# Performance work log

Measured on AMD Instinct MI355X. Metric: run time of the kernel, lower is better.

## Reference

```python
import jax, jax.numpy as jnp
import numpy as np

B, T, C = 128, 256, 384
H, HD = 8, 48          # num_heads, head_dim
WINDOW = 64

def setup_inputs() -> dict:
    key = jax.random.key(0)
    ks = jax.random.split(key, 5)
    return {
        "x": jax.random.normal(ks[0], (B, T, C), dtype=jnp.float32),
        "W_qkv": jax.random.normal(ks[1], (C, 3 * C), dtype=jnp.float32) * (1.0 / np.sqrt(C)),
        "b_qkv": jax.random.normal(ks[2], (3 * C,), dtype=jnp.float32) * 0.02,
        "W_proj": jax.random.normal(ks[3], (C, C), dtype=jnp.float32) * (1.0 / np.sqrt(C)),
        "b_proj": jax.random.normal(ks[4], (C,), dtype=jnp.float32) * 0.02,
        "gate": jnp.ones((C,), dtype=jnp.float32),
    }

def reference(x, W_qkv, b_qkv, W_proj, b_proj, gate):
    Bx, Tx, Cx = x.shape
    qkv = x @ W_qkv + b_qkv                                   # [B,T,3C]
    q, k, v = jnp.split(qkv, 3, axis=-1)
    q = q.reshape(Bx, Tx, H, HD).transpose(0, 2, 1, 3)        # [B,H,T,hd]
    k = k.reshape(Bx, Tx, H, HD).transpose(0, 2, 1, 3)
    v = v.reshape(Bx, Tx, H, HD).transpose(0, 2, 1, 3)
    scale = 1.0 / np.sqrt(HD).astype(np.float32)
    att = jnp.einsum("bhqd,bhkd->bhqk", q, k) * scale        # [B,H,T,T]
    idx = jnp.arange(Tx)
    causal = idx[:, None] >= idx[None, :]                     # lower-tri
    local = jnp.abs(idx[None, :] - idx[:, None]) <= WINDOW
    mask = (causal & local)[None, None, :, :]
    att = jnp.where(mask, att, -jnp.inf)
    att = jax.nn.softmax(att, axis=-1)
    out = jnp.einsum("bhqk,bhkd->bhqd", att, v)               # [B,H,T,hd]
    out = out.transpose(0, 2, 1, 3).reshape(Bx, Tx, Cx)       # [B,T,C]
    return (out * gate) @ W_proj + b_proj
```

## Files before the change

kernel.cpp:

```cpp
#include <hip/hip_runtime.h>
#include <hip/hip_bf16.h>

typedef __attribute__((ext_vector_type(8))) short bf16x8;
typedef __attribute__((ext_vector_type(4))) float floatx4;

#define NB 128
#define NT 256
#define NC 384
#define NH 8
#define ND 48
#define CPLANE (128 * 8 * 256 * 48)

static __device__ __forceinline__ unsigned short f2bf(float f) {
  __hip_bfloat16 h = __float2bfloat16(f);
  return __builtin_bit_cast(unsigned short, h);
}

static __device__ __forceinline__ void gload16(const unsigned short* g, unsigned short* l) {
  __builtin_amdgcn_global_load_lds(
      (const __attribute__((address_space(1))) void*)g,
      (__attribute__((address_space(3))) void*)l, 16, 0, 0);
}

__global__ __launch_bounds__(256) void k_prep(const float* __restrict__ x,
                                              const float* __restrict__ Wq,
                                              const float* __restrict__ Wp,
                                              const float* __restrict__ gate,
                                              unsigned short* __restrict__ xbf,
                                              unsigned short* __restrict__ WqT,
                                              unsigned short* __restrict__ WpT) {
  const int blk = blockIdx.x;
  const int t = threadIdx.x;
  if (blk < 144) {
    __shared__ float T[64][65];
    const float* src;
    unsigned short* dst;
    int N, kt, nt;
    const bool isWp = (blk >= 108);
    if (!isWp) { src = Wq; dst = WqT; N = 1152; kt = blk / 18; nt = blk % 18; }
    else { int b2 = blk - 108; src = Wp; dst = WpT; N = 384; kt = b2 / 6; nt = b2 % 6; }
    const int k0 = kt * 64, n0 = nt * 64;
    const int r = t >> 2, c = (t & 3) * 16;
    const float* s = src + (size_t)(k0 + r) * N + n0 + c;
#pragma unroll
    for (int i = 0; i < 4; ++i) *(float4*)&T[r][c + i * 4] = ((const float4*)s)[i];
    __syncthreads();
    float gv[16];
    if (isWp) {
#pragma unroll
      for (int i = 0; i < 4; ++i) *(float4*)&gv[i * 4] = ((const float4*)(gate + k0 + c))[i];
    } else {
#pragma unroll
      for (int i = 0; i < 16; ++i) gv[i] = 1.f;
    }
    unsigned short o[16];
#pragma unroll
    for (int i = 0; i < 16; ++i) o[i] = f2bf(T[c + i][r] * gv[i]);
    unsigned short* dp = dst + (size_t)(n0 + r) * 384 + k0 + c;
    *(bf16x8*)dp = *(bf16x8*)&o[0];
    *(bf16x8*)(dp + 8) = *(bf16x8*)&o[8];
  } else {
    const int n8 = (NB * NT * NC) / 8;
    int idx = (blk - 144) * 256 + t;
    const int stride = (gridDim.x - 144) * 256;
    for (; idx < n8; idx += stride) {
      const float* s = x + (size_t)idx * 8;
      float v[8];
      *(float4*)&v[0] = ((const float4*)s)[0];
      *(float4*)&v[4] = ((const float4*)s)[1];
      bf16x8 p;
#pragma unroll
      for (int i = 0; i < 8; ++i) p[i] = f2bf(v[i]);
      *(bf16x8*)(xbf + (size_t)idx * 8) = p;
    }
  }
}

#define STAGE_G(Ag, Bg, k0, buf)                                                     \
  {                                                                                  \
    const int r0_ = (lane >> 2), sw0_ = 8 * ((lane & 3) ^ ((r0_ >> 1) & 3));         \
    const int r1_ = r0_ + 16,    sw1_ = 8 * ((lane & 3) ^ ((r1_ >> 1) & 3));         \
    gload16((Ag) + (size_t)r0_ * 384 + (k0) + sw0_, As + (buf)*4096 + (w * 32) * 32);  \
    gload16((Ag) + (size_t)r1_ * 384 + (k0) + sw1_, As + (buf)*4096 + (w * 32 + 16) * 32); \
    gload16((Bg) + (size_t)r0_ * 384 + (k0) + sw0_, Bs + (buf)*4096 + (w * 32) * 32);  \
    gload16((Bg) + (size_t)r1_ * 384 + (k0) + sw1_, Bs + (buf)*4096 + (w * 32 + 16) * 32); \
  }

#define GEMM_PIPE(Ag, Bg)                                                            \
  STAGE_G(Ag, Bg, 0, 0);                                                             \
  STAGE_G(Ag, Bg, 32, 1);                                                            \
  _Pragma("unroll") for (int t_ = 0; t_ < 12; ++t_) {                                \
    if (t_ < 11) asm volatile("s_waitcnt vmcnt(4)" ::: "memory");                    \
    else         asm volatile("s_waitcnt vmcnt(0)" ::: "memory");                    \
    __builtin_amdgcn_s_barrier();                                                    \
    if (t_ < 10) STAGE_G(Ag, Bg, (t_ + 2) * 32, (t_ + 2) % 3);                       \
    const unsigned short* Ac_ = As + (t_ % 3) * 4096;                                \
    const unsigned short* Bc_ = Bs + (t_ % 3) * 4096;                                \
    bf16x8 a_[4], b_[4];                                                             \
    _Pragma("unroll") for (int mt = 0; mt < 4; ++mt) {                               \
      const int R = wm * 64 + mt * 16 + lq;                                          \
      a_[mt] = *(const bf16x8*)&Ac_[R * 32 + 8 * (lg ^ ((R >> 1) & 3))];             \
    }                                                                                \
    _Pragma("unroll") for (int nt = 0; nt < 4; ++nt) {                               \
      const int R = wn * 64 + nt * 16 + lq;                                          \
      b_[nt] = *(const bf16x8*)&Bc_[R * 32 + 8 * (lg ^ ((R >> 1) & 3))];             \
    }                                                                                \
    _Pragma("unroll") for (int mt = 0; mt < 4; ++mt)                                 \
      _Pragma("unroll") for (int nt = 0; nt < 4; ++nt)                               \
        acc[mt][nt] = __builtin_amdgcn_mfma_f32_16x16x32_bf16(a_[mt], b_[nt], acc[mt][nt], 0, 0, 0); \
  }

__global__ __launch_bounds__(256) void k_qkv(const unsigned short* __restrict__ xb,
                                             const unsigned short* __restrict__ WqT,
                                             const float* __restrict__ bq,
                                             unsigned short* __restrict__ qkv) {
  __shared__ __align__(16) unsigned short As[3 * 4096];
  __shared__ __align__(16) unsigned short Bs[3 * 4096];
  const int t = threadIdx.x, lane = t & 63, w = t >> 6;
  const int wm = w >> 1, wn = w & 1;
  const int lq = lane & 15, lg = lane >> 4;
  const int swz = (blockIdx.x & 7) * 288 + (blockIdx.x >> 3);
  const int m0 = (swz / 9) * 128, n0 = (swz % 9) * 128;
  const int comp = n0 / 384;
  const unsigned short* Ag = xb + (size_t)(m0 + w * 32) * 384;
  const unsigned short* Bg = WqT + (size_t)(n0 + w * 32) * 384;
  floatx4 acc[4][4] = {};

  GEMM_PIPE(Ag, Bg);

  __builtin_amdgcn_s_barrier();
  unsigned short* Ew = ((w < 2) ? As : Bs) + 2 * 4096 + (w & 1) * 2048;
#pragma unroll
  for (int p = 0; p < 4; ++p) {
#pragma unroll
    for (int nt = 0; nt < 4; ++nt) {
      const float bias = bq[n0 + wn * 64 + nt * 16 + lq];
#pragma unroll
      for (int j = 0; j < 4; ++j)
        Ew[(lg * 4 + j) * 72 + nt * 16 + lq] = f2bf(acc[p][nt][j] + bias);
    }
    asm volatile("s_waitcnt lgkmcnt(0)" ::: "memory");
    __builtin_amdgcn_sched_barrier(0);
#pragma unroll
    for (int cc = 0; cc < 2; ++cc) {
      const int c = cc * 64 + lane;
      const int r16 = c >> 3, k8 = c & 7;
      bf16x8 v = *(const bf16x8*)&Ew[r16 * 72 + k8 * 8];
      const int lc = n0 - comp * 384 + wn * 64 + k8 * 8;
      const int hh = lc / 48, d0 = lc - hh * 48;
      const int R = m0 + wm * 64 + p * 16 + r16;
      *(bf16x8*)(qkv + (size_t)comp * CPLANE +
                 (((size_t)((R >> 8) * 8 + hh) * 256 + (R & 255)) * 48 + d0)) = v;
    }
    asm volatile("s_waitcnt lgkmcnt(0)" ::: "memory");
    __builtin_amdgcn_sched_barrier(0);
  }
}

__global__ __launch_bounds__(256) void k_proj(const unsigned short* __restrict__ A,
                                              const unsigned short* __restrict__ WpT,
                                              const float* __restrict__ bp,
                                              float* __restrict__ out) {
  __shared__ __align__(16) unsigned short As[3 * 4096];
  __shared__ __align__(16) unsigned short Bs[3 * 4096];
  const int t = threadIdx.x, lane = t & 63, w = t >> 6;
  const int wm = w >> 1, wn = w & 1;
  const int lq = lane & 15, lg = lane >> 4;
  const int swz = (blockIdx.x & 7) * 96 + (blockIdx.x >> 3);
  const int m0 = (swz / 3) * 128, n0 = (swz % 3) * 128;
  const unsigned short* Ag = A + (size_t)(m0 + w * 32) * 384;
  const unsigned short* Bg = WpT + (size_t)(n0 + w * 32) * 384;
  floatx4 acc[4][4] = {};

  GEMM_PIPE(Ag, Bg);

#pragma unroll
  for (int nt = 0; nt < 4; ++nt) {
    const int col = n0 + wn * 64 + nt * 16 + lq;
    const float bias = bp[col];
#pragma unroll
    for (int mt = 0; mt < 4; ++mt)
#pragma unroll
      for (int j = 0; j < 4; ++j) {
        const int row = m0 + wm * 64 + mt * 16 + lg * 4 + j;
        out[(size_t)row * 384 + col] = acc[mt][nt][j] + bias;
      }
  }
}

__global__ __launch_bounds__(256) void k_attn(const unsigned short* __restrict__ qkv,
                                              unsigned short* __restrict__ attg) {
  __shared__ __align__(16) unsigned short Ks[128 * 72];
  __shared__ __align__(16) unsigned short Vt[48 * 152];
  __shared__ __align__(16) unsigned short Ps[4 * 16 * 104];
  const int t = threadIdx.x;
  const int blk = blockIdx.x;
  const int tile = blk & 3;
  const int bh = blk >> 2;
  const int b = bh >> 3, h = bh & 7;
  const int base = tile * 64;
  const size_t kvoff = (size_t)bh * NT * ND;
  const unsigned short* qptr = qkv + kvoff;
  const unsigned short* kptr = qkv + (size_t)CPLANE + kvoff;
  const unsigned short* vptr = qkv + (size_t)2 * CPLANE + kvoff;

  if (t < 48) {
    bf16x8 z = {};
    *(bf16x8*)&Vt[t * 152 + 128] = z;
    *(bf16x8*)&Vt[t * 152 + 136] = z;
  }
  if (t < 128) {
    const int r = t, ka = base - 64 + r;
    unsigned short* dst = &Ks[r * 72];
    if (ka >= 0) {
      const unsigned short* src = kptr + (size_t)ka * ND;
#pragma unroll
      for (int i = 0; i < 6; ++i) *(bf16x8*)(dst + i * 8) = *(const bf16x8*)(src + i * 8);
      bf16x8 z = {};
      *(bf16x8*)(dst + 48) = z;
      *(bf16x8*)(dst + 56) = z;
    } else {
      bf16x8 z = {};
#pragma unroll
      for (int i = 0; i < 8; ++i) *(bf16x8*)(dst + i * 8) = z;
    }
  } else {
    const int r = t - 128, ka = base - 64 + r;
    if (ka >= 0) {
      const unsigned short* src = vptr + (size_t)ka * ND;
      bf16x8 vv[6];
#pragma unroll
      for (int i = 0; i < 6; ++i) vv[i] = *(const bf16x8*)(src + i * 8);
#pragma unroll
      for (int i = 0; i < 6; ++i)
#pragma unroll
        for (int j = 0; j < 8; ++j)
          Vt[(i * 8 + j) * 152 + r] = (unsigned short)vv[i][j];
    } else {
#pragma unroll
      for (int d = 0; d < 48; ++d) Vt[d * 152 + r] = 0;
    }
  }
  __syncthreads();

  const int lane = t & 63, w = t >> 6;
  const int lq = lane & 15, lg = lane >> 4;
  const int qs = base + w * 16;

  const unsigned short* qrow = qptr + (size_t)(qs + lq) * ND;
  bf16x8 aq0 = *(const bf16x8*)(qrow + lg * 8);
  bf16x8 aq1 = {};
  if (lg < 2) aq1 = *(const bf16x8*)(qrow + 32 + lg * 8);

  floatx4 s[5];
#pragma unroll
  for (int kt = 0; kt < 5; ++kt) {
    const unsigned short* kr = &Ks[(w * 16 + kt * 16 + lq) * 72];
    bf16x8 kb0 = *(const bf16x8*)(kr + lg * 8);
    bf16x8 kb1 = *(const bf16x8*)(kr + 32 + lg * 8);
    floatx4 z = {};
    z = __builtin_amdgcn_mfma_f32_16x16x32_bf16(aq0, kb0, z, 0, 0, 0);
    z = __builtin_amdgcn_mfma_f32_16x16x32_bf16(aq1, kb1, z, 0, 0, 0);
    s[kt] = z;
  }

  const float scale = 0.14433756729740643f;
  floatx4 pj[5];
#pragma unroll
  for (int j = 0; j < 4; ++j) {
    const int qa = qs + lg * 4 + j;
    float mx = -1e30f;
    float sv[5];
    bool ok[5];
#pragma unroll
    for (int kt = 0; kt < 5; ++kt) {
      const int ka = base - 64 + w * 16 + kt * 16 + lq;
      sv[kt] = s[kt][j] * scale;
      ok[kt] = (ka >= 0) && (ka <= qa) && (qa - ka <= 64);
      if (ok[kt]) mx = fmaxf(mx, sv[kt]);
    }
#pragma unroll
    for (int dd = 1; dd < 16; dd <<= 1) mx = fmaxf(mx, __shfl_xor(mx, dd));
    float sum = 0.f;
#pragma unroll
    for (int kt = 0; kt < 5; ++kt) {
      float p = ok[kt] ? __expf(sv[kt] - mx) : 0.f;
      pj[kt][j] = p;
      sum += p;
    }
#pragma unroll
    for (int dd = 1; dd < 16; dd <<= 1) sum += __shfl_xor(sum, dd);
    const float inv = 1.f / sum;
#pragma unroll
    for (int kt = 0; kt < 5; ++kt) pj[kt][j] *= inv;
  }

  unsigned short* pw = &Ps[w * 16 * 104];
#pragma unroll
  for (int kt = 0; kt < 5; ++kt)
#pragma unroll
    for (int j = 0; j < 4; ++j)
      pw[(lg * 4 + j) * 104 + kt * 16 + lq] = f2bf(pj[kt][j]);
#pragma unroll
  for (int j = 0; j < 4; ++j) pw[lq * 104 + 80 + lg * 4 + j] = 0;

  floatx4 o[3] = {};
#pragma unroll
  for (int c = 0; c < 3; ++c) {
    bf16x8 ap = *(const bf16x8*)&pw[lq * 104 + c * 32 + lg * 8];
#pragma unroll
    for (int nt = 0; nt < 3; ++nt) {
      bf16x8 av = *(const bf16x8*)&Vt[(nt * 16 + lq) * 152 + w * 16 + c * 32 + lg * 8];
      o[nt] = __builtin_amdgcn_mfma_f32_16x16x32_bf16(ap, av, o[nt], 0, 0, 0);
    }
  }
#pragma unroll
  for (int nt = 0; nt < 3; ++nt) {
    const int d = nt * 16 + lq;
    const int c = h * ND + d;
#pragma unroll
    for (int j = 0; j < 4; ++j) {
      const int tt = qs + lg * 4 + j;
      attg[((size_t)b * NT + tt) * NC + c] = f2bf(o[nt][j]);
    }
  }
}

extern "C" void kernel_launch(void* const* d_in, const int* in_sizes, int n_in,
                              void* d_out, int out_size, void* d_ws, size_t ws_size,
                              hipStream_t stream) {
  const float* x    = (const float*)d_in[0];
  const float* Wq   = (const float*)d_in[1];
  const float* bq   = (const float*)d_in[2];
  const float* Wp   = (const float*)d_in[3];
  const float* bp   = (const float*)d_in[4];
  const float* gate = (const float*)d_in[5];

  const size_t nx = (size_t)NB * NT * NC;
  unsigned short* attg = (unsigned short*)d_ws;
  unsigned short* xbf  = attg + nx;
  unsigned short* qkvp = xbf + nx;
  unsigned short* WqT  = qkvp + (size_t)3 * CPLANE;
  unsigned short* WpT  = WqT + (size_t)384 * 1152;
  float* out = (float*)d_out;

  k_prep<<<dim3(1680), 256, 0, stream>>>(x, Wq, Wp, gate, xbf, WqT, WpT);
  k_qkv<<<dim3(2304), 256, 0, stream>>>(xbf, WqT, bq, qkvp);
  k_attn<<<dim3(4096), 256, 0, stream>>>(qkvp, attg);
  k_proj<<<dim3(768), 256, 0, stream>>>(attg, WpT, bp, out);
}
```

Before: 113.3 us.

## Process whole sequence per (batch,head) block in attention, loading K/V once

The attention kernel now launches one block per (batch, head) instead of four per (batch, head) query tile. The full 256-row K and transposed V are loaded into shared memory once, and the block loops over four 64-row query segments. This removes the overlapping K/V window reloads and the zero-padding branches of the old 128-row staging. In exchange, shared memory per block grows and there are a quarter as many blocks, which lowers parallelism and occupancy.

```diff
diff --git a/kernel.cpp b/kernel.cpp
--- a/kernel.cpp
+++ b/kernel.cpp
@@ -190,139 +190,128 @@
 
 __global__ __launch_bounds__(256) void k_attn(const unsigned short* __restrict__ qkv,
                                               unsigned short* __restrict__ attg) {
-  __shared__ __align__(16) unsigned short Ks[128 * 72];
-  __shared__ __align__(16) unsigned short Vt[48 * 152];
+  __shared__ __align__(16) unsigned short Ks[256 * 72];
+  __shared__ __align__(16) unsigned short Vt[48 * 280];
   __shared__ __align__(16) unsigned short Ps[4 * 16 * 104];
   const int t = threadIdx.x;
-  const int blk = blockIdx.x;
-  const int tile = blk & 3;
-  const int bh = blk >> 2;
+  const int bh = blockIdx.x;
   const int b = bh >> 3, h = bh & 7;
-  const int base = tile * 64;
   const size_t kvoff = (size_t)bh * NT * ND;
   const unsigned short* qptr = qkv + kvoff;
   const unsigned short* kptr = qkv + (size_t)CPLANE + kvoff;
   const unsigned short* vptr = qkv + (size_t)2 * CPLANE + kvoff;
 
-  if (t < 48) {
+  {
+    const unsigned short* src = kptr + (size_t)t * ND;
+    unsigned short* dst = &Ks[t * 72];
+#pragma unroll
+    for (int i = 0; i < 6; ++i) *(bf16x8*)(dst + i * 8) = *(const bf16x8*)(src + i * 8);
     bf16x8 z = {};
-    *(bf16x8*)&Vt[t * 152 + 128] = z;
-    *(bf16x8*)&Vt[t * 152 + 136] = z;
-  }
-  if (t < 128) {
-    const int r = t, ka = base - 64 + r;
-    unsigned short* dst = &Ks[r * 72];
-    if (ka >= 0) {
-      const unsigned short* src = kptr + (size_t)ka * ND;
-#pragma unroll
-      for (int i = 0; i < 6; ++i) *(bf16x8*)(dst + i * 8) = *(const bf16x8*)(src + i * 8);
-      bf16x8 z = {};
-      *(bf16x8*)(dst + 48) = z;
-      *(bf16x8*)(dst + 56) = z;
-    } else {
-      bf16x8 z = {};
-#pragma unroll
-      for (int i = 0; i < 8; ++i) *(bf16x8*)(dst + i * 8) = z;
-    }
-  } else {
-    const int r = t - 128, ka = base - 64 + r;
-    if (ka >= 0) {
-      const unsigned short* src = vptr + (size_t)ka * ND;
-      bf16x8 vv[6];
-#pragma unroll
-      for (int i = 0; i < 6; ++i) vv[i] = *(const bf16x8*)(src + i * 8);
-#pragma unroll
-      for (int i = 0; i < 6; ++i)
-#pragma unroll
-        for (int j = 0; j < 8; ++j)
-          Vt[(i * 8 + j) * 152 + r] = (unsigned short)vv[i][j];
-    } else {
-#pragma unroll
-      for (int d = 0; d < 48; ++d) Vt[d * 152 + r] = 0;
-    }
+    *(bf16x8*)(dst + 48) = z;
+    *(bf16x8*)(dst + 56) = z;
+  }
+  {
+    const unsigned short* src = vptr + (size_t)t * ND;
+    bf16x8 vv[6];
+#pragma unroll
+    for (int i = 0; i < 6; ++i) vv[i] = *(const bf16x8*)(src + i * 8);
+#pragma unroll
+    for (int i = 0; i < 6; ++i)
+#pragma unroll
+      for (int j = 0; j < 8; ++j)
+        Vt[(i * 8 + j) * 280 + t] = (unsigned short)vv[i][j];
+  }
+  if (t < 144) {
+    bf16x8 z = {};
+    *(bf16x8*)&Vt[(t / 3) * 280 + 256 + (t % 3) * 8] = z;
   }
   __syncthreads();
 
   const int lane = t & 63, w = t >> 6;
   const int lq = lane & 15, lg = lane >> 4;
-  const int qs = base + w * 16;
-
-  const unsigned short* qrow = qptr + (size_t)(qs + lq) * ND;
-  bf16x8 aq0 = *(const bf16x8*)(qrow + lg * 8);
-  bf16x8 aq1 = {};
-  if (lg < 2) aq1 = *(const bf16x8*)(qrow + 32 + lg * 8);
-
-  floatx4 s[5];
-#pragma unroll
-  for (int kt = 0; kt < 5; ++kt) {
-    const unsigned short* kr = &Ks[(w * 16 + kt * 16 + lq) * 72];
-    bf16x8 kb0 = *(const bf16x8*)(kr + lg * 8);
-    bf16x8 kb1 = *(const bf16x8*)(kr + 32 + lg * 8);
-    floatx4 z = {};
-    z = __builtin_amdgcn_mfma_f32_16x16x32_bf16(aq0, kb0, z, 0, 0, 0);
-    z = __builtin_amdgcn_mfma_f32_16x16x32_bf16(aq1, kb1, z, 0, 0, 0);
-    s[kt] = z;
-  }
-
   const float scale = 0.14433756729740643f;
-  floatx4 pj[5];
-#pragma unroll
-  for (int j = 0; j < 4; ++j) {
-    const int qa = qs + lg * 4 + j;
-    float mx = -1e30f;
-    float sv[5];
-    bool ok[5];
+  unsigned short* pw = &Ps[w * 16 * 104];
+
+  for (int s = 0; s < 4; ++s) {
+    const int qs = s * 64 + w * 16;
+    const int kstart = (qs >= 64) ? (qs - 64) : 0;
+
+    const unsigned short* qrow = qptr + (size_t)(qs + lq) * ND;
+    bf16x8 aq0 = *(const bf16x8*)(qrow + lg * 8);
+    bf16x8 aq1 = {};
+    if (lg < 2) aq1 = *(const bf16x8*)(qrow + 32 + lg * 8);
+
+    floatx4 sv4[5];
 #pragma unroll
     for (int kt = 0; kt < 5; ++kt) {
-      const int ka = base - 64 + w * 16 + kt * 16 + lq;
-      sv[kt] = s[kt][j] * scale;
-      ok[kt] = (ka >= 0) && (ka <= qa) && (qa - ka <= 64);
-      if (ok[kt]) mx = fmaxf(mx, sv[kt]);
-    }
-#pragma unroll
-    for (int dd = 1; dd < 16; dd <<= 1) mx = fmaxf(mx, __shfl_xor(mx, dd));
-    float sum = 0.f;
-#pragma unroll
-    for (int kt = 0; kt < 5; ++kt) {
-      float p = ok[kt] ? __expf(sv[kt] - mx) : 0.f;
-      pj[kt][j] = p;
-      sum += p;
-    }
-#pragma unroll
-    for (int dd = 1; dd < 16; dd <<= 1) sum += __shfl_xor(sum, dd);
-    const float inv = 1.f / sum;
-#pragma unroll
-    for (int kt = 0; kt < 5; ++kt) pj[kt][j] *= inv;
-  }
-
-  unsigned short* pw = &Ps[w * 16 * 104];
-#pragma unroll
-  for (int kt = 0; kt < 5; ++kt)
-#pragma unroll
-    for (int j = 0; j < 4; ++j)
-      pw[(lg * 4 + j) * 104 + kt * 16 + lq] = f2bf(pj[kt][j]);
-#pragma unroll
-  for (int j = 0; j < 4; ++j) pw[lq * 104 + 80 + lg * 4 + j] = 0;
-
-  floatx4 o[3] = {};
-#pragma unroll
-  for (int c = 0; c < 3; ++c) {
-    bf16x8 ap = *(const bf16x8*)&pw[lq * 104 + c * 32 + lg * 8];
+      const unsigned short* kr = &Ks[(kstart + kt * 16 + lq) * 72];
+      bf16x8 kb0 = *(const bf16x8*)(kr + lg * 8);
+      bf16x8 kb1 = *(const bf16x8*)(kr + 32 + lg * 8);
+      floatx4 z = {};
+      z = __builtin_amdgcn_mfma_f32_16x16x32_bf16(aq0, kb0, z, 0, 0, 0);
+      z = __builtin_amdgcn_mfma_f32_16x16x32_bf16(aq1, kb1, z, 0, 0, 0);
+      sv4[kt] = z;
+    }
+
+    floatx4 pj[5];
+#pragma unroll
+    for (int j = 0; j < 4; ++j) {
+      const int qa = qs + lg * 4 + j;
+      float mx = -1e30f;
+      float sv[5];
+      bool ok[5];
+#pragma unroll
+      for (int kt = 0; kt < 5; ++kt) {
+        const int ka = kstart + kt * 16 + lq;
+        sv[kt] = sv4[kt][j] * scale;
+        ok[kt] = (ka <= qa) && (qa - ka <= 64);
+        if (ok[kt]) mx = fmaxf(mx, sv[kt]);
+      }
+#pragma unroll
+      for (int dd = 1; dd < 16; dd <<= 1) mx = fmaxf(mx, __shfl_xor(mx, dd));
+      float sum = 0.f;
+#pragma unroll
+      for (int kt = 0; kt < 5; ++kt) {
+        float p = ok[kt] ? __expf(sv[kt] - mx) : 0.f;
+        pj[kt][j] = p;
+        sum += p;
+      }
+#pragma unroll
+      for (int dd = 1; dd < 16; dd <<= 1) sum += __shfl_xor(sum, dd);
+      const float inv = 1.f / sum;
+#pragma unroll
+      for (int kt = 0; kt < 5; ++kt) pj[kt][j] *= inv;
+    }
+
+#pragma unroll
+    for (int kt = 0; kt < 5; ++kt)
+#pragma unroll
+      for (int j = 0; j < 4; ++j)
+        pw[(lg * 4 + j) * 104 + kt * 16 + lq] = f2bf(pj[kt][j]);
+#pragma unroll
+    for (int j = 0; j < 4; ++j) pw[lq * 104 + 80 + lg * 4 + j] = 0;
+
+    floatx4 o[3] = {};
+#pragma unroll
+    for (int c = 0; c < 3; ++c) {
+      bf16x8 ap = *(const bf16x8*)&pw[lq * 104 + c * 32 + lg * 8];
+#pragma unroll
+      for (int nt = 0; nt < 3; ++nt) {
+        bf16x8 av = *(const bf16x8*)&Vt[(nt * 16 + lq) * 280 + kstart + c * 32 + lg * 8];
+        o[nt] = __builtin_amdgcn_mfma_f32_16x16x32_bf16(ap, av, o[nt], 0, 0, 0);
+      }
+    }
 #pragma unroll
     for (int nt = 0; nt < 3; ++nt) {
-      bf16x8 av = *(const bf16x8*)&Vt[(nt * 16 + lq) * 152 + w * 16 + c * 32 + lg * 8];
-      o[nt] = __builtin_amdgcn_mfma_f32_16x16x32_bf16(ap, av, o[nt], 0, 0, 0);
-    }
-  }
-#pragma unroll
-  for (int nt = 0; nt < 3; ++nt) {
-    const int d = nt * 16 + lq;
-    const int c = h * ND + d;
-#pragma unroll
-    for (int j = 0; j < 4; ++j) {
-      const int tt = qs + lg * 4 + j;
-      attg[((size_t)b * NT + tt) * NC + c] = f2bf(o[nt][j]);
-    }
+      const int d = nt * 16 + lq;
+      const int c = h * ND + d;
+#pragma unroll
+      for (int j = 0; j < 4; ++j) {
+        const int tt = qs + lg * 4 + j;
+        attg[((size_t)b * NT + tt) * NC + c] = f2bf(o[nt][j]);
+      }
+    }
+    __syncthreads();
   }
 }
 
@@ -346,6 +335,6 @@
 
   k_prep<<<dim3(1680), 256, 0, stream>>>(x, Wq, Wp, gate, xbf, WqT, WpT);
   k_qkv<<<dim3(2304), 256, 0, stream>>>(xbf, WqT, bq, qkvp);
-  k_attn<<<dim3(4096), 256, 0, stream>>>(qkvp, attg);
+  k_attn<<<dim3(1024), 256, 0, stream>>>(qkvp, attg);
   k_proj<<<dim3(768), 256, 0, stream>>>(attg, WpT, bp, out);
 }
```

Result: faster. 110.9 us (-2.1%).
